# Optimization experiments

Measured on AMD Instinct MI355X. Metric: run time of the kernel, lower is better.

## Reference

```python
import jax, jax.numpy as jnp
import numpy as np

H, D = 2, 64          # heads, hidden_dim per head
HD = H * D            # 128
N_NODES = 50000
N_EDGES = 800000
N_GRAPHS = 64
IN_CH, EDGE_DIM, N_CLASSES = 2, 1, 30


def _tconv(x, src, dst, Wq, bq, Wk, bk, Wv, bv, We, Ws, bs):
    """PyG TransformerConv (concat=True, root_weight=True, beta=False)."""
    n = x.shape[0]
    q = (x @ Wq + bq).reshape(n, H, D)
    k = (x @ Wk + bk).reshape(n, H, D)
    v = (x @ Wv + bv).reshape(n, H, D)
    # edge embedding (lin_edge has no bias in PyG)
    return _attend(q, k, v, x @ Ws + bs, src, dst, We, n)


def _attend(q, k, v, skip, src, dst, We_e, n):
    kj = k[src] + We_e            # [E,H,D]
    vj = v[src] + We_e
    logits = (q[dst] * kj).sum(-1) / jnp.sqrt(jnp.asarray(D, q.dtype))  # [E,H]
    m = jax.ops.segment_max(logits, dst, num_segments=n)
    m = jnp.where(jnp.isfinite(m), m, jnp.zeros_like(m))
    ex = jnp.exp(logits - m[dst])
    denom = jax.ops.segment_sum(ex, dst, num_segments=n)
    alpha = ex / (denom[dst] + 1e-16)                                   # segment softmax
    agg = jax.ops.segment_sum(alpha[..., None] * vj, dst, num_segments=n)
    return agg.reshape(n, HD) + skip


def _forward(x, edge_index, edge_attr, batch,
             l0_Wq, l0_bq, l0_Wk, l0_bk, l0_Wv, l0_bv, l0_We, l0_Ws, l0_bs,
             l1_Wq, l1_bq, l1_Wk, l1_bk, l1_Wv, l1_bv, l1_We, l1_Ws, l1_bs,
             cW1, cb1, cW2, cb2):
    src, dst = edge_index[0], edge_index[1]
    e0 = (edge_attr @ l0_We).reshape(-1, H, D)
    e1 = (edge_attr @ l1_We).reshape(-1, H, D)
    n = x.shape[0]

    h = _attend((x @ l0_Wq + l0_bq).reshape(n, H, D),
                (x @ l0_Wk + l0_bk).reshape(n, H, D),
                (x @ l0_Wv + l0_bv).reshape(n, H, D),
                x @ l0_Ws + l0_bs, src, dst, e0, n)
    h = jax.nn.relu(h)
    h = _attend((h @ l1_Wq + l1_bq).reshape(n, H, D),
                (h @ l1_Wk + l1_bk).reshape(n, H, D),
                (h @ l1_Wv + l1_bv).reshape(n, H, D),
                h @ l1_Ws + l1_bs, src, dst, e1, n)
    h = jax.nn.relu(h)

    # global_mean_pool over graphs
    sums = jax.ops.segment_sum(h, batch, num_segments=N_GRAPHS)
    cnt = jax.ops.segment_sum(jnp.ones((n,), h.dtype), batch, num_segments=N_GRAPHS)
    g = sums / jnp.maximum(cnt, 1.0)[:, None]                           # [G, 128]

    return jax.nn.relu(g @ cW1 + cb1) @ cW2 + cb2                       # [G, 30]


def setup_inputs() -> dict:
    key = jax.random.key(0)
    ks = jax.random.split(key, 40)
    it = iter(ks)

    def lin(k, fan_in, fan_out):
        s = 1.0 / np.sqrt(fan_in)
        return jax.random.uniform(k, (fan_in, fan_out), jnp.float32, -s, s)

    inp = {
        'x': jax.random.normal(next(it), (N_NODES, IN_CH), jnp.float32),
        'edge_index': jax.random.randint(next(it), (2, N_EDGES), 0, N_NODES),
        'edge_attr': jax.random.normal(next(it), (N_EDGES, EDGE_DIM), jnp.float32),
        'batch': jnp.sort(jax.random.randint(next(it), (N_NODES,), 0, N_GRAPHS)),
    }
    for li, cin in (('l0', IN_CH), ('l1', HD)):
        for nm in ('Wq', 'Wk', 'Wv'):
            inp[f'{li}_{nm}'] = lin(next(it), cin, HD)
            inp[f'{li}_{nm.replace("W", "b")}'] = jax.random.uniform(
                next(it), (HD,), jnp.float32, -1 / np.sqrt(cin), 1 / np.sqrt(cin))
        inp[f'{li}_We'] = lin(next(it), EDGE_DIM, HD)
        inp[f'{li}_Ws'] = lin(next(it), cin, HD)
        inp[f'{li}_bs'] = jax.random.uniform(next(it), (HD,), jnp.float32,
                                             -1 / np.sqrt(cin), 1 / np.sqrt(cin))
    inp['cW1'] = lin(next(it), HD, 128)
    inp['cb1'] = jax.random.uniform(next(it), (128,), jnp.float32, -1 / np.sqrt(HD), 1 / np.sqrt(HD))
    inp['cW2'] = lin(next(it), 128, N_CLASSES)
    inp['cb2'] = jax.random.uniform(next(it), (N_CLASSES,), jnp.float32, -1 / np.sqrt(128), 1 / np.sqrt(128))
    return inp


def reference(x, edge_index, edge_attr, batch,
              l0_Wq, l0_bq, l0_Wk, l0_bk, l0_Wv, l0_bv, l0_We, l0_Ws, l0_bs,
              l1_Wq, l1_bq, l1_Wk, l1_bk, l1_Wv, l1_bv, l1_We, l1_Ws, l1_bs,
              cW1, cb1, cW2, cb2):
    return _forward(x, edge_index, edge_attr, batch,
                    l0_Wq, l0_bq, l0_Wk, l0_bk, l0_Wv, l0_bv, l0_We, l0_Ws, l0_bs,
                    l1_Wq, l1_bq, l1_Wk, l1_bk, l1_Wv, l1_bv, l1_We, l1_Ws, l1_bs,
                    cW1, cb1, cW2, cb2)
```

## Files before the change

### kernel.cpp

```cpp
#include <hip/hip_runtime.h>
#include <hip/hip_fp16.h>
#include <cstdint>
#include <cstddef>

#define HD 128

typedef short bf16x8 __attribute__((ext_vector_type(8)));
typedef float f32x4 __attribute__((ext_vector_type(4)));
typedef _Float16 h2f __attribute__((ext_vector_type(2)));

__device__ __forceinline__ h2f bits_to_h2(int v) {
    union { int i; h2f h; } u; u.i = v; return u.h;
}

#if __has_builtin(__builtin_amdgcn_fdot2)
#define DOT2(a, b) __builtin_amdgcn_fdot2((a), (b), 0.f, false)
#else
#define DOT2(a, b) fmaf((float)(a).x, (float)(b).x, (float)(a).y * (float)(b).y)
#endif

__device__ __forceinline__ unsigned short f2bf(float f) {
    unsigned int u = __float_as_uint(f);
    u += 0x7fff + ((u >> 16) & 1);
    return (unsigned short)(u >> 16);
}
__device__ __forceinline__ float bf2f(unsigned short h) {
    return __uint_as_float(((unsigned int)h) << 16);
}

template<int CTRL>
__device__ __forceinline__ float dpp_add(float x) {
    int y = __builtin_amdgcn_update_dpp(0, __float_as_int(x), CTRL, 0xF, 0xF, true);
    return x + __int_as_float(y);
}
__device__ __forceinline__ float half_reduce(float x) {
    x = dpp_add<0xB1>(x);
    x = dpp_add<0x4E>(x);
    x = dpp_add<0x124>(x);
    x = dpp_add<0x128>(x);
    x += __shfl_xor(x, 16, 64);
    return x;
}
__device__ __forceinline__ float wave_reduce(float x) {
    x = half_reduce(x);
    x += __shfl_xor(x, 32, 64);
    return x;
}

__device__ __forceinline__ void edge_pair(
    float& m, float& s, float& Sea, float2& acc, float cqwe, h2f q,
    int2 rawA, float aA, int2 rawB, float aB)
{
    h2f kA = bits_to_h2(rawA.x), vA = bits_to_h2(rawA.y);
    h2f kB = bits_to_h2(rawB.x), vB = bits_to_h2(rawB.y);
    float lA = fmaf(aA, cqwe, half_reduce(DOT2(q, kA)));
    float lB = fmaf(aB, cqwe, half_reduce(DOT2(q, kB)));
    float nm = fmaxf(fmaxf(m, lA), lB);
    float sc = __expf(m - nm);
    float eA = __expf(lA - nm);
    float eB = __expf(lB - nm);
    s   = fmaf(s, sc, eA + eB);
    Sea = fmaf(Sea, sc, fmaf(eA, aA, eB * aB));
    acc.x = fmaf(acc.x, sc, fmaf(eA, (float)vA.x, eB * (float)vB.x));
    acc.y = fmaf(acc.y, sc, fmaf(eA, (float)vA.y, eB * (float)vB.y));
    m = nm;
}
__device__ __forceinline__ void edge_single(
    float& m, float& s, float& Sea, float2& acc, float cqwe, h2f q,
    int2 rawA, float aA)
{
    h2f kA = bits_to_h2(rawA.x), vA = bits_to_h2(rawA.y);
    float lg = fmaf(aA, cqwe, half_reduce(DOT2(q, kA)));
    float nm = fmaxf(m, lg);
    float sc = __expf(m - nm);
    float ex = __expf(lg - nm);
    s   = fmaf(s, sc, ex);
    Sea = fmaf(Sea, sc, ex * aA);
    acc.x = fmaf(acc.x, sc, ex * (float)vA.x);
    acc.y = fmaf(acc.y, sc, ex * (float)vA.y);
    m = nm;
}

__global__ __launch_bounds__(256) void hist_kernel(
    const int* __restrict__ dst, int* __restrict__ cnt, int E)
{
    int e = blockIdx.x * 256 + threadIdx.x;
    if (e < E) atomicAdd(&cnt[dst[e]], 1);
}

__global__ __launch_bounds__(256) void scanA_kernel(
    const int* __restrict__ cnt, int* __restrict__ row_ptr,
    int* __restrict__ bsum, int n)
{
    __shared__ int sdata[256];
    int t = threadIdx.x;
    int base = blockIdx.x * 512 + 2 * t;
    int a = (base < n) ? cnt[base] : 0;
    int b = (base + 1 < n) ? cnt[base + 1] : 0;
    int local = a + b;
    sdata[t] = local;
    __syncthreads();
    #pragma unroll
    for (int off = 1; off < 256; off <<= 1) {
        int val = (t >= off) ? sdata[t - off] : 0;
        __syncthreads();
        sdata[t] += val;
        __syncthreads();
    }
    int excl = sdata[t] - local;
    if (base < n)     row_ptr[base] = excl;
    if (base + 1 < n) row_ptr[base + 1] = excl + a;
    if (t == 255) bsum[blockIdx.x] = sdata[255];
}

__global__ __launch_bounds__(256) void scanB_kernel(
    const int* __restrict__ bsum, int* __restrict__ boff, int B)
{
    __shared__ int sdata[256];
    int t = threadIdx.x;
    int local = (t < B) ? bsum[t] : 0;
    sdata[t] = local;
    __syncthreads();
    #pragma unroll
    for (int off = 1; off < 256; off <<= 1) {
        int val = (t >= off) ? sdata[t - off] : 0;
        __syncthreads();
        sdata[t] += val;
        __syncthreads();
    }
    if (t < B) boff[t] = sdata[t] - local;
}

__global__ __launch_bounds__(256) void scanC_kernel(
    int* __restrict__ row_ptr, int* __restrict__ cursor,
    const int* __restrict__ boff, int n, int E)
{
    int t = threadIdx.x;
    int base = blockIdx.x * 512 + 2 * t;
    int off = boff[blockIdx.x];
    if (base + 1 < n) {
        int2 v = *(int2*)&row_ptr[base];
        v.x += off; v.y += off;
        *(int2*)&row_ptr[base] = v;
        *(int2*)&cursor[base]  = v;
    } else if (base < n) {
        int v = row_ptr[base] + off;
        row_ptr[base] = v; cursor[base] = v;
    }
    if (blockIdx.x == 0 && t == 0) row_ptr[n] = E;
}

__global__ __launch_bounds__(256) void scatter_kernel(
    const int* __restrict__ dst, const int* __restrict__ src,
    const float* __restrict__ eattr, int* __restrict__ cursor,
    int2* __restrict__ epack, int E)
{
    int e = blockIdx.x * 256 + threadIdx.x;
    if (e < E) {
        int pos = atomicAdd(&cursor[dst[e]], 1);
        epack[pos] = make_int2(src[e], __float_as_int(eattr[e]));
    }
}

__global__ __launch_bounds__(128) void coef0_kernel(
    const float* __restrict__ Wq, const float* __restrict__ bq,
    const float* __restrict__ Wk, const float* __restrict__ bk,
    const float* __restrict__ We, float* __restrict__ coef)
{
    int w = threadIdx.x >> 6, l = threadIdx.x & 63;
    int j = w * 64 + l;
    float q0 = Wq[j], q1 = Wq[HD + j], qb = bq[j];
    float kv[4] = {Wk[j], Wk[HD + j], bk[j], We[j]};
    #pragma unroll
    for (int t = 0; t < 4; ++t) {
        float m0 = wave_reduce(kv[t] * q0);
        float m1 = wave_reduce(kv[t] * q1);
        float m2 = wave_reduce(kv[t] * qb);
        if (l == 0) {
            coef[w * 12 + t * 3 + 0] = m0 * 0.125f;
            coef[w * 12 + t * 3 + 1] = m1 * 0.125f;
            coef[w * 12 + t * 3 + 2] = m2 * 0.125f;
        }
    }
}

__global__ __launch_bounds__(256) void attn0a_kernel(
    const float* __restrict__ x, const float* __restrict__ coef,
    const int2* __restrict__ epack, const int* __restrict__ row_ptr,
    float4* __restrict__ S, int n)
{
    int i = blockIdx.x * 256 + threadIdx.x;
    if (i >= n) return;
    float C[24];
    #pragma unroll
    for (int t = 0; t < 24; ++t) C[t] = coef[t];
    float x0 = x[2 * i], x1 = x[2 * i + 1];
    float c0A = fmaf(x1, C[1],  fmaf(x0, C[0],  C[2]));
    float c1A = fmaf(x1, C[4],  fmaf(x0, C[3],  C[5]));
    float cbA = fmaf(x1, C[7],  fmaf(x0, C[6],  C[8]));
    float cwA = fmaf(x1, C[10], fmaf(x0, C[9],  C[11]));
    float c0B = fmaf(x1, C[13], fmaf(x0, C[12], C[14]));
    float c1B = fmaf(x1, C[16], fmaf(x0, C[15], C[17]));
    float cbB = fmaf(x1, C[19], fmaf(x0, C[18], C[20]));
    float cwB = fmaf(x1, C[22], fmaf(x0, C[21], C[23]));

    int p0 = row_ptr[i], p1 = row_ptr[i + 1];
    float mA = -INFINITY, sA = 0.f, SxA = 0.f, SyA = 0.f, SeA = 0.f;
    float mB = -INFINITY, sB = 0.f, SxB = 0.f, SyB = 0.f, SeB = 0.f;

    int2 epn = (p0 < p1) ? epack[p0] : make_int2(0, 0);
    for (int p = p0; p < p1; ++p) {
        int2 ep = epn;
        if (p + 1 < p1) epn = epack[p + 1];
        float ea = __int_as_float(ep.y);
        float2 xs = *(const float2*)&x[2 * ep.x];
        float lgA = fmaf(ea, cwA, fmaf(xs.y, c1A, fmaf(xs.x, c0A, cbA)));
        float lgB = fmaf(ea, cwB, fmaf(xs.y, c1B, fmaf(xs.x, c0B, cbB)));
        {
            float nm = fmaxf(mA, lgA);
            float sc = __expf(mA - nm);
            float ex = __expf(lgA - nm);
            sA  = fmaf(sA,  sc, ex);
            SxA = fmaf(SxA, sc, ex * xs.x);
            SyA = fmaf(SyA, sc, ex * xs.y);
            SeA = fmaf(SeA, sc, ex * ea);
            mA = nm;
        }
        {
            float nm = fmaxf(mB, lgB);
            float sc = __expf(mB - nm);
            float ex = __expf(lgB - nm);
            sB  = fmaf(sB,  sc, ex);
            SxB = fmaf(SxB, sc, ex * xs.x);
            SyB = fmaf(SyB, sc, ex * xs.y);
            SeB = fmaf(SeB, sc, ex * ea);
            mB = nm;
        }
    }
    S[(size_t)i * 2]     = make_float4(sA, SxA, SyA, SeA);
    S[(size_t)i * 2 + 1] = make_float4(sB, SxB, SyB, SeB);
}

__global__ __launch_bounds__(256) void attn_kernel(
    const __half* __restrict__ qh, const __half* __restrict__ kvh,
    const __half* __restrict__ sh, const float* __restrict__ We,
    const int2* __restrict__ epack, const int* __restrict__ row_ptr,
    __half2* __restrict__ outh, int n)
{
    int i = blockIdx.x * 4 + (threadIdx.x >> 6);
    if (i >= n) return;
    int l = threadIdx.x & 63;
    const int2* kv8 = (const int2*)kvh;
    const int* qraw = (const int*)qh;
    const __half2* sh2 = (const __half2*)sh;
    h2f q = bits_to_h2(qraw[(size_t)i * 64 + l]);
    float2 we = *(const float2*)&We[2 * l];
    float cqwe = half_reduce(fmaf((float)q.x, we.x, (float)q.y * we.y));
    int p0 = __builtin_amdgcn_readfirstlane(row_ptr[i]);
    int p1 = __builtin_amdgcn_readfirstlane(row_ptr[i + 1]);

    float m = -INFINITY, s = 0.f, Sea = 0.f;
    float2 acc = make_float2(0.f, 0.f);

    int2 kv0 = {}, kv1 = {}, kv2 = {}, kv3 = {};
    float ea0 = 0.f, ea1 = 0.f, ea2 = 0.f, ea3 = 0.f;

#define LD1(t, idx) do { if ((idx) < p1) { int2 ep_ = epack[idx]; \
    ea##t = __int_as_float(ep_.y); kv##t = kv8[(size_t)ep_.x * 64 + l]; } } while (0)

    LD1(0, p0); LD1(1, p0 + 1); LD1(2, p0 + 2); LD1(3, p0 + 3);

    int p = p0;
    for (; p + 3 < p1; p += 4) {
        int2 c0 = kv0, c1 = kv1, c2 = kv2, c3 = kv3;
        float a0 = ea0, a1 = ea1, a2 = ea2, a3 = ea3;
        LD1(0, p + 4); LD1(1, p + 5); LD1(2, p + 6); LD1(3, p + 7);
        edge_pair(m, s, Sea, acc, cqwe, q, c0, a0, c1, a1);
        edge_pair(m, s, Sea, acc, cqwe, q, c2, a2, c3, a3);
    }
    int rem = p1 - p;
    if (rem >= 2) edge_pair(m, s, Sea, acc, cqwe, q, kv0, ea0, kv1, ea1);
    if (rem == 1)      edge_single(m, s, Sea, acc, cqwe, q, kv0, ea0);
    else if (rem == 3) edge_single(m, s, Sea, acc, cqwe, q, kv2, ea2);

    float inv = 1.f / (s + 1e-16f);
    float2 skp = __half22float2(sh2[(size_t)i * 64 + l]);
    float rx = fmaxf(fmaf(fmaf(Sea, we.x, acc.x), inv, skp.x), 0.f);
    float ry = fmaxf(fmaf(fmaf(Sea, we.y, acc.y), inv, skp.y), 0.f);
    outh[(size_t)i * 64 + l] = __floats2half2_rn(rx, ry);
}

__global__ __launch_bounds__(256) void pack_kernel(
    const float* __restrict__ Wq, const float* __restrict__ Wk,
    const float* __restrict__ Wv, const float* __restrict__ Ws,
    const float* __restrict__ bq, const float* __restrict__ bk,
    const float* __restrict__ bv, const float* __restrict__ bs,
    unsigned short* __restrict__ Wph, unsigned short* __restrict__ Wpl,
    float* __restrict__ bias_cat)
{
    int id = blockIdx.x * 256 + threadIdx.x;
    if (id < 65536) {
        int j = id & 7, lane = (id >> 3) & 63, ks = (id >> 9) & 3, gnt = id >> 11;
        int k = ks * 32 + (lane >> 4) * 8 + j;
        int ncol = gnt * 16 + (lane & 15);
        int mat = ncol >> 7, d = ncol & 127;
        const float* W = (mat == 0) ? Wq : (mat == 1) ? Wk : (mat == 2) ? Wv : Ws;
        float w = W[k * HD + d];
        unsigned short hi = f2bf(w);
        Wph[id] = hi;
        Wpl[id] = f2bf(w - bf2f(hi));
    }
    if (id < 512) {
        int mat = id >> 7, d = id & 127;
        const float* b = (mat == 0) ? bq : (mat == 1) ? bk : (mat == 2) ? bv : bs;
        bias_cat[id] = b[d];
    }
}

__global__ __launch_bounds__(256) void lin1_mfma(
    const float* __restrict__ x, const float4* __restrict__ S0,
    const float* __restrict__ l0Wv, const float* __restrict__ l0bv,
    const float* __restrict__ l0We,
    const float* __restrict__ l0Ws, const float* __restrict__ l0bs,
    const unsigned short* __restrict__ Wph, const unsigned short* __restrict__ Wpl,
    const float* __restrict__ bias_cat,
    __half* __restrict__ qh, __half* __restrict__ kvh, __half* __restrict__ sh,
    int n)
{
    __shared__ float As[128 * 128];
    int tid = threadIdx.x;
    int row0 = blockIdx.x * 128;

    {
        int c4 = tid & 31;
        int c0 = c4 * 4;
        int rb = tid >> 5;
        int hh = c4 >> 4;
        float4 wv0 = *(const float4*)&l0Wv[c0];
        float4 wv1 = *(const float4*)&l0Wv[HD + c0];
        float4 bv4 = *(const float4*)&l0bv[c0];
        float4 we4 = *(const float4*)&l0We[c0];
        float4 ws0 = *(const float4*)&l0Ws[c0];
        float4 ws1 = *(const float4*)&l0Ws[HD + c0];
        float4 bs4 = *(const float4*)&l0bs[c0];
        #pragma unroll
        for (int it = 0; it < 16; ++it) {
            int r = it * 8 + rb;
            float4 av = make_float4(0.f, 0.f, 0.f, 0.f);
            if (row0 + r < n) {
                float2 xr = *(const float2*)&x[2 * (size_t)(row0 + r)];
                float4 Sv = S0[(size_t)(row0 + r) * 2 + hh];
                float inv = 1.f / (Sv.x + 1e-16f);
                float n0 = fmaf(wv0.x, Sv.y, fmaf(wv1.x, Sv.z, fmaf(bv4.x, Sv.x, we4.x * Sv.w)));
                float n1 = fmaf(wv0.y, Sv.y, fmaf(wv1.y, Sv.z, fmaf(bv4.y, Sv.x, we4.y * Sv.w)));
                float n2 = fmaf(wv0.z, Sv.y, fmaf(wv1.z, Sv.z, fmaf(bv4.z, Sv.x, we4.z * Sv.w)));
                float n3 = fmaf(wv0.w, Sv.y, fmaf(wv1.w, Sv.z, fmaf(bv4.w, Sv.x, we4.w * Sv.w)));
                av.x = fmaxf(fmaf(n0, inv, fmaf(xr.y, ws1.x, fmaf(xr.x, ws0.x, bs4.x))), 0.f);
                av.y = fmaxf(fmaf(n1, inv, fmaf(xr.y, ws1.y, fmaf(xr.x, ws0.y, bs4.y))), 0.f);
                av.z = fmaxf(fmaf(n2, inv, fmaf(xr.y, ws1.z, fmaf(xr.x, ws0.z, bs4.z))), 0.f);
                av.w = fmaxf(fmaf(n3, inv, fmaf(xr.y, ws1.w, fmaf(xr.x, ws0.w, bs4.w))), 0.f);
            }
            int sl = c4 ^ (r & 7);
            *(float4*)&As[r * 128 + sl * 4] = av;
        }
    }
    __syncthreads();

    int wave = tid >> 6, lane = tid & 63;
    int m = lane & 15, quad = lane >> 4;

    bf16x8 ah[2][4], al[2][4];
    #pragma unroll
    for (int sub = 0; sub < 2; ++sub) {
        int r = wave * 32 + sub * 16 + m;
        const float* base = &As[r * 128];
        int sw = r & 7;
        #pragma unroll
        for (int ks = 0; ks < 4; ++ks) {
            int i40 = (ks * 8 + quad * 2) ^ sw;
            int i41 = (ks * 8 + quad * 2 + 1) ^ sw;
            float4 x0 = *(const float4*)&base[i40 * 4];
            float4 x1 = *(const float4*)&base[i41 * 4];
            float v[8] = {x0.x, x0.y, x0.z, x0.w, x1.x, x1.y, x1.z, x1.w};
            #pragma unroll
            for (int j = 0; j < 8; ++j) {
                unsigned short hi = f2bf(v[j]);
                ah[sub][ks][j] = (short)hi;
                al[sub][ks][j] = (short)f2bf(v[j] - bf2f(hi));
            }
        }
    }
    __syncthreads();

    const bf16x8* PH = (const bf16x8*)Wph;
    const bf16x8* PL = (const bf16x8*)Wpl;
    __half2* qh2 = (__half2*)qh;
    __half2* sh2 = (__half2*)sh;
    __half*  kvS = (__half*)As;

    bf16x8 bhA[4], blA[4], bhB[4], blB[4];
    #pragma unroll
    for (int ks = 0; ks < 4; ++ks) {
        bhA[ks] = PH[ks * 64 + lane];
        blA[ks] = PL[ks * 64 + lane];
    }

    for (int gnt = 0; gnt < 32; ++gnt) {
        if (gnt + 1 < 32) {
            #pragma unroll
            for (int ks = 0; ks < 4; ++ks) {
                bhB[ks] = PH[((gnt + 1) * 4 + ks) * 64 + lane];
                blB[ks] = PL[((gnt + 1) * 4 + ks) * 64 + lane];
            }
        }
        f32x4 acc0 = {0.f, 0.f, 0.f, 0.f};
        f32x4 acc1 = {0.f, 0.f, 0.f, 0.f};
        #pragma unroll
        for (int ks = 0; ks < 4; ++ks) {
            acc0 = __builtin_amdgcn_mfma_f32_16x16x32_bf16(ah[0][ks], bhA[ks], acc0, 0, 0, 0);
            acc1 = __builtin_amdgcn_mfma_f32_16x16x32_bf16(ah[1][ks], bhA[ks], acc1, 0, 0, 0);
            acc0 = __builtin_amdgcn_mfma_f32_16x16x32_bf16(ah[0][ks], blA[ks], acc0, 0, 0, 0);
            acc1 = __builtin_amdgcn_mfma_f32_16x16x32_bf16(ah[1][ks], blA[ks], acc1, 0, 0, 0);
            acc0 = __builtin_amdgcn_mfma_f32_16x16x32_bf16(al[0][ks], bhA[ks], acc0, 0, 0, 0);
            acc1 = __builtin_amdgcn_mfma_f32_16x16x32_bf16(al[1][ks], bhA[ks], acc1, 0, 0, 0);
        }
        int ocol = gnt * 16 + m;
        int d = ocol & 127;
        float bias = bias_cat[ocol];
        bool iskv = (gnt >= 8) && (gnt < 24);
        if (!iskv) {
            bool isq = (gnt < 8);
            __half2* dst = isq ? qh2 : sh2;
            float osc = isq ? 0.125f : 1.0f;
            bool evenl = (m & 1) == 0;
            #pragma unroll
            for (int sub = 0; sub < 2; ++sub) {
                f32x4 acc = sub ? acc1 : acc0;
                #pragma unroll
                for (int reg = 0; reg < 4; ++reg) {
                    int orow = row0 + wave * 32 + sub * 16 + quad * 4 + reg;
                    float val = (acc[reg] + bias) * osc;
                    float other = __shfl_xor(val, 1, 64);
                    if (orow < n && evenl)
                        dst[(size_t)orow * 64 + (d >> 1)] = __floats2half2_rn(val, other);
                }
            }
        } else {
            int slot = 4 * (d >> 1) + (d & 1) + ((gnt >= 16) ? 2 : 0);
            #pragma unroll
            for (int sub = 0; sub < 2; ++sub) {
                f32x4 acc = sub ? acc1 : acc0;
                #pragma unroll
                for (int reg = 0; reg < 4; ++reg) {
                    int row_l = wave * 32 + sub * 16 + quad * 4 + reg;
                    kvS[row_l * 256 + slot] = __float2half(acc[reg] + bias);
                }
            }
        }
        #pragma unroll
        for (int ks = 0; ks < 4; ++ks) { bhA[ks] = bhB[ks]; blA[ks] = blB[ks]; }
    }

    __syncthreads();
    const float4* kvS4 = (const float4*)kvS;
    float4* kvh4 = (float4*)kvh;
    #pragma unroll
    for (int it = 0; it < 16; ++it) {
        int idx = it * 256 + tid;
        int row = idx >> 5, c4 = idx & 31;
        if (row0 + row < n)
            kvh4[(size_t)(row0 + row) * 32 + c4] = kvS4[row * 32 + c4];
    }
}

__global__ __launch_bounds__(128) void pool_kernel(
    const __half* __restrict__ h, const int* __restrict__ batch,
    float* __restrict__ gsums, int n)
{
    __shared__ int sb[64];
    int i0 = blockIdx.x * 64;
    int d = threadIdx.x;
    int iend = i0 + 64; if (iend > n) iend = n;
    int csize = iend - i0;
    if (d < csize) sb[d] = batch[i0 + d];
    __syncthreads();
    if (csize <= 0) return;
    float local = 0.f;
    int cur = sb[0];
    for (int i = i0; i < iend; ++i) {
        int g = sb[i - i0];
        if (g != cur) {
            atomicAdd(&gsums[(size_t)cur * HD + d], local);
            local = 0.f; cur = g;
        }
        local += __half2float(h[(size_t)i * HD + d]);
    }
    atomicAdd(&gsums[(size_t)cur * HD + d], local);
}

__global__ __launch_bounds__(128) void cls_kernel(
    const float* __restrict__ gsums, const int* __restrict__ batch,
    const float* __restrict__ cW1, const float* __restrict__ cb1,
    const float* __restrict__ cW2, const float* __restrict__ cb2,
    float* __restrict__ out, int n)
{
    __shared__ float g[128];
    __shared__ float t[128];
    int gi = blockIdx.x, j = threadIdx.x;
    int lo = 0, hi = n;
    while (lo < hi) { int mid = (lo + hi) >> 1; if (batch[mid] < gi) lo = mid + 1; else hi = mid; }
    int start = lo;
    lo = start; hi = n;
    while (lo < hi) { int mid = (lo + hi) >> 1; if (batch[mid] < gi + 1) lo = mid + 1; else hi = mid; }
    float c = fmaxf((float)(lo - start), 1.0f);
    g[j] = gsums[(size_t)gi * HD + j] / c;
    __syncthreads();
    float a = cb1[j];
    for (int k = 0; k < 128; ++k) a = fmaf(g[k], cW1[k * 128 + j], a);
    t[j] = fmaxf(a, 0.f);
    __syncthreads();
    if (j < 30) {
        float a2 = cb2[j];
        for (int k = 0; k < 128; ++k) a2 = fmaf(t[k], cW2[k * 30 + j], a2);
        out[gi * 30 + j] = a2;
    }
}

extern "C" void kernel_launch(void* const* d_in, const int* in_sizes, int n_in,
                              void* d_out, int out_size, void* d_ws, size_t ws_size,
                              hipStream_t stream)
{
    const float* x     = (const float*)d_in[0];
    const int*   ei    = (const int*)d_in[1];
    const float* eattr = (const float*)d_in[2];
    const int*   batch = (const int*)d_in[3];
    const float* l0_Wq = (const float*)d_in[4];
    const float* l0_bq = (const float*)d_in[5];
    const float* l0_Wk = (const float*)d_in[6];
    const float* l0_bk = (const float*)d_in[7];
    const float* l0_Wv = (const float*)d_in[8];
    const float* l0_bv = (const float*)d_in[9];
    const float* l0_We = (const float*)d_in[10];
    const float* l0_Ws = (const float*)d_in[11];
    const float* l0_bs = (const float*)d_in[12];
    const float* l1_Wq = (const float*)d_in[13];
    const float* l1_bq = (const float*)d_in[14];
    const float* l1_Wk = (const float*)d_in[15];
    const float* l1_bk = (const float*)d_in[16];
    const float* l1_Wv = (const float*)d_in[17];
    const float* l1_bv = (const float*)d_in[18];
    const float* l1_We = (const float*)d_in[19];
    const float* l1_Ws = (const float*)d_in[20];
    const float* l1_bs = (const float*)d_in[21];
    const float* cW1   = (const float*)d_in[22];
    const float* cb1   = (const float*)d_in[23];
    const float* cW2   = (const float*)d_in[24];
    const float* cb2   = (const float*)d_in[25];

    int n = in_sizes[0] / 2;
    int E = in_sizes[2];
    int G = out_size / 30;
    int B = (n + 511) / 512;

    size_t nd = (size_t)n * HD;
    __half* h1    = (__half*)d_ws;
    __half* qh    = h1 + nd;
    __half* sh    = qh + nd;
    __half* kvh   = sh + nd;
    float* bias_cat = (float*)(kvh + (size_t)n * 256);
    unsigned short* Wph = (unsigned short*)(bias_cat + 512);
    unsigned short* Wpl = Wph + 65536;
    float* coef   = (float*)(Wpl + 65536);
    float4* S0    = (float4*)(coef + 32);
    int2* epack   = (int2*)(S0 + (size_t)n * 2);
    int* cnt      = (int*)(epack + E);
    int* row_ptr  = cnt + n;
    int* cursor   = row_ptr + n + 2;
    int* bsum     = cursor + n;
    int* boff     = bsum + 256;
    float* gsums  = (float*)(boff + 256);

    const int* srcI = ei;
    const int* dstI = ei + E;

    hipMemsetAsync(cnt, 0, (size_t)n * sizeof(int), stream);
    hipMemsetAsync(gsums, 0, (size_t)G * HD * sizeof(float), stream);

    hist_kernel<<<(E + 255) / 256, 256, 0, stream>>>(dstI, cnt, E);
    scanA_kernel<<<B, 256, 0, stream>>>(cnt, row_ptr, bsum, n);
    scanB_kernel<<<1, 256, 0, stream>>>(bsum, boff, B);
    scanC_kernel<<<B, 256, 0, stream>>>(row_ptr, cursor, boff, n, E);
    scatter_kernel<<<(E + 255) / 256, 256, 0, stream>>>(dstI, srcI, eattr, cursor, epack, E);

    pack_kernel<<<256, 256, 0, stream>>>(l1_Wq, l1_Wk, l1_Wv, l1_Ws,
                                         l1_bq, l1_bk, l1_bv, l1_bs,
                                         Wph, Wpl, bias_cat);
    coef0_kernel<<<1, 128, 0, stream>>>(l0_Wq, l0_bq, l0_Wk, l0_bk, l0_We, coef);

    attn0a_kernel<<<(n + 255) / 256, 256, 0, stream>>>(
        x, coef, epack, row_ptr, S0, n);

    lin1_mfma<<<(n + 127) / 128, 256, 0, stream>>>(
        x, S0, l0_Wv, l0_bv, l0_We, l0_Ws, l0_bs,
        Wph, Wpl, bias_cat, qh, kvh, sh, n);
    attn_kernel<<<(n + 3) / 4, 256, 0, stream>>>(
        qh, kvh, sh, l1_We, epack, row_ptr, (__half2*)h1, n);

    pool_kernel<<<(n + 63) / 64, 128, 0, stream>>>(h1, batch, gsums, n);
    cls_kernel<<<G, 128, 0, stream>>>(gsums, batch, cW1, cb1, cW2, cb2,
                                      (float*)d_out, n);
}
```

Measured before the change: 359.6 us.

## Fuse setup kernels, split attn0a edges across lane pairs, shrink lin1 tile

Folds the coef0 computation, the cnt zeroing and the weight packing into one pack_kernel, and replaces both memsets. scanB is merged into scanC, with each block re-scanning the block sums itself. attn0a now gives each node two threads that walk alternate edges and merge their online-softmax states with shuffles, which raises parallelism for the low-occupancy gather loop. lin1_mfma uses 64-row tiles instead of 128, halving shared memory and doubling the grid for occupancy, and it zeroes gsums in block 0. The costs are redundant scan work per block and less MFMA reuse of the B fragments per tile.

```diff
diff --git a/kernel.cpp b/kernel.cpp
--- a/kernel.cpp
+++ b/kernel.cpp
@@ -81,6 +81,56 @@
     m = nm;
 }
 
+__global__ __launch_bounds__(256) void pack_kernel(
+    const float* __restrict__ Wq, const float* __restrict__ Wk,
+    const float* __restrict__ Wv, const float* __restrict__ Ws,
+    const float* __restrict__ bq, const float* __restrict__ bk,
+    const float* __restrict__ bv, const float* __restrict__ bs,
+    const float* __restrict__ l0Wq, const float* __restrict__ l0bq,
+    const float* __restrict__ l0Wk, const float* __restrict__ l0bk,
+    const float* __restrict__ l0We,
+    unsigned short* __restrict__ Wph, unsigned short* __restrict__ Wpl,
+    float* __restrict__ bias_cat, float* __restrict__ coef,
+    int* __restrict__ cnt, int n)
+{
+    int tid = threadIdx.x;
+    int id = blockIdx.x * 256 + tid;
+    if (id < 65536) {
+        int j = id & 7, lane = (id >> 3) & 63, ks = (id >> 9) & 3, gnt = id >> 11;
+        int k = ks * 32 + (lane >> 4) * 8 + j;
+        int ncol = gnt * 16 + (lane & 15);
+        int mat = ncol >> 7, d = ncol & 127;
+        const float* W = (mat == 0) ? Wq : (mat == 1) ? Wk : (mat == 2) ? Wv : Ws;
+        float w = W[k * HD + d];
+        unsigned short hi = f2bf(w);
+        Wph[id] = hi;
+        Wpl[id] = f2bf(w - bf2f(hi));
+    }
+    if (id < 512) {
+        int mat = id >> 7, d = id & 127;
+        const float* b = (mat == 0) ? bq : (mat == 1) ? bk : (mat == 2) ? bv : bs;
+        bias_cat[id] = b[d];
+    }
+    if (id < n) cnt[id] = 0;
+    if (blockIdx.x == 256 && tid < 128) {
+        int w = tid >> 6, l = tid & 63;
+        int j = w * 64 + l;
+        float q0 = l0Wq[j], q1 = l0Wq[HD + j], qb = l0bq[j];
+        float kv[4] = {l0Wk[j], l0Wk[HD + j], l0bk[j], l0We[j]};
+        #pragma unroll
+        for (int t = 0; t < 4; ++t) {
+            float m0 = wave_reduce(kv[t] * q0);
+            float m1 = wave_reduce(kv[t] * q1);
+            float m2 = wave_reduce(kv[t] * qb);
+            if (l == 0) {
+                coef[w * 12 + t * 3 + 0] = m0 * 0.125f;
+                coef[w * 12 + t * 3 + 1] = m1 * 0.125f;
+                coef[w * 12 + t * 3 + 2] = m2 * 0.125f;
+            }
+        }
+    }
+}
+
 __global__ __launch_bounds__(256) void hist_kernel(
     const int* __restrict__ dst, int* __restrict__ cnt, int E)
 {
@@ -113,12 +163,13 @@
     if (t == 255) bsum[blockIdx.x] = sdata[255];
 }
 
-__global__ __launch_bounds__(256) void scanB_kernel(
-    const int* __restrict__ bsum, int* __restrict__ boff, int B)
+__global__ __launch_bounds__(256) void scanC_kernel(
+    int* __restrict__ row_ptr, int* __restrict__ cursor,
+    const int* __restrict__ bsum, int n, int E, int B)
 {
     __shared__ int sdata[256];
     int t = threadIdx.x;
-    int local = (t < B) ? bsum[t] : 0;
+    int local = (t < B && t < (int)blockIdx.x) ? bsum[t] : 0;
     sdata[t] = local;
     __syncthreads();
     #pragma unroll
@@ -128,16 +179,8 @@
         sdata[t] += val;
         __syncthreads();
     }
-    if (t < B) boff[t] = sdata[t] - local;
-}
-
-__global__ __launch_bounds__(256) void scanC_kernel(
-    int* __restrict__ row_ptr, int* __restrict__ cursor,
-    const int* __restrict__ boff, int n, int E)
-{
-    int t = threadIdx.x;
+    int off = sdata[255];
     int base = blockIdx.x * 512 + 2 * t;
-    int off = boff[blockIdx.x];
     if (base + 1 < n) {
         int2 v = *(int2*)&row_ptr[base];
         v.x += off; v.y += off;
@@ -162,34 +205,13 @@
     }
 }
 
-__global__ __launch_bounds__(128) void coef0_kernel(
-    const float* __restrict__ Wq, const float* __restrict__ bq,
-    const float* __restrict__ Wk, const float* __restrict__ bk,
-    const float* __restrict__ We, float* __restrict__ coef)
-{
-    int w = threadIdx.x >> 6, l = threadIdx.x & 63;
-    int j = w * 64 + l;
-    float q0 = Wq[j], q1 = Wq[HD + j], qb = bq[j];
-    float kv[4] = {Wk[j], Wk[HD + j], bk[j], We[j]};
-    #pragma unroll
-    for (int t = 0; t < 4; ++t) {
-        float m0 = wave_reduce(kv[t] * q0);
-        float m1 = wave_reduce(kv[t] * q1);
-        float m2 = wave_reduce(kv[t] * qb);
-        if (l == 0) {
-            coef[w * 12 + t * 3 + 0] = m0 * 0.125f;
-            coef[w * 12 + t * 3 + 1] = m1 * 0.125f;
-            coef[w * 12 + t * 3 + 2] = m2 * 0.125f;
-        }
-    }
-}
-
 __global__ __launch_bounds__(256) void attn0a_kernel(
     const float* __restrict__ x, const float* __restrict__ coef,
     const int2* __restrict__ epack, const int* __restrict__ row_ptr,
     float4* __restrict__ S, int n)
 {
-    int i = blockIdx.x * 256 + threadIdx.x;
+    int gid = blockIdx.x * 256 + threadIdx.x;
+    int i = gid >> 1, pr = gid & 1;
     if (i >= n) return;
     float C[24];
     #pragma unroll
@@ -208,10 +230,11 @@
     float mA = -INFINITY, sA = 0.f, SxA = 0.f, SyA = 0.f, SeA = 0.f;
     float mB = -INFINITY, sB = 0.f, SxB = 0.f, SyB = 0.f, SeB = 0.f;
 
-    int2 epn = (p0 < p1) ? epack[p0] : make_int2(0, 0);
-    for (int p = p0; p < p1; ++p) {
+    int p = p0 + pr;
+    int2 epn = (p < p1) ? epack[p] : make_int2(0, 0);
+    for (; p < p1; p += 2) {
         int2 ep = epn;
-        if (p + 1 < p1) epn = epack[p + 1];
+        if (p + 2 < p1) epn = epack[p + 2];
         float ea = __int_as_float(ep.y);
         float2 xs = *(const float2*)&x[2 * ep.x];
         float lgA = fmaf(ea, cwA, fmaf(xs.y, c1A, fmaf(xs.x, c0A, cbA)));
@@ -237,8 +260,30 @@
             mB = nm;
         }
     }
-    S[(size_t)i * 2]     = make_float4(sA, SxA, SyA, SeA);
-    S[(size_t)i * 2 + 1] = make_float4(sB, SxB, SyB, SeB);
+    {
+        float mO = __shfl_xor(mA, 1, 64);
+        float mM = fmaxf(mA, mO);
+        float e = (mA > -INFINITY) ? __expf(mA - mM) : 0.f;
+        sA *= e; SxA *= e; SyA *= e; SeA *= e;
+        sA  += __shfl_xor(sA, 1, 64);
+        SxA += __shfl_xor(SxA, 1, 64);
+        SyA += __shfl_xor(SyA, 1, 64);
+        SeA += __shfl_xor(SeA, 1, 64);
+    }
+    {
+        float mO = __shfl_xor(mB, 1, 64);
+        float mM = fmaxf(mB, mO);
+        float e = (mB > -INFINITY) ? __expf(mB - mM) : 0.f;
+        sB *= e; SxB *= e; SyB *= e; SeB *= e;
+        sB  += __shfl_xor(sB, 1, 64);
+        SxB += __shfl_xor(SxB, 1, 64);
+        SyB += __shfl_xor(SyB, 1, 64);
+        SeB += __shfl_xor(SeB, 1, 64);
+    }
+    if (pr == 0) {
+        S[(size_t)i * 2]     = make_float4(sA, SxA, SyA, SeA);
+        S[(size_t)i * 2 + 1] = make_float4(sB, SxB, SyB, SeB);
+    }
 }
 
 __global__ __launch_bounds__(256) void attn_kernel(
@@ -290,33 +335,6 @@
     outh[(size_t)i * 64 + l] = __floats2half2_rn(rx, ry);
 }
 
-__global__ __launch_bounds__(256) void pack_kernel(
-    const float* __restrict__ Wq, const float* __restrict__ Wk,
-    const float* __restrict__ Wv, const float* __restrict__ Ws,
-    const float* __restrict__ bq, const float* __restrict__ bk,
-    const float* __restrict__ bv, const float* __restrict__ bs,
-    unsigned short* __restrict__ Wph, unsigned short* __restrict__ Wpl,
-    float* __restrict__ bias_cat)
-{
-    int id = blockIdx.x * 256 + threadIdx.x;
-    if (id < 65536) {
-        int j = id & 7, lane = (id >> 3) & 63, ks = (id >> 9) & 3, gnt = id >> 11;
-        int k = ks * 32 + (lane >> 4) * 8 + j;
-        int ncol = gnt * 16 + (lane & 15);
-        int mat = ncol >> 7, d = ncol & 127;
-        const float* W = (mat == 0) ? Wq : (mat == 1) ? Wk : (mat == 2) ? Wv : Ws;
-        float w = W[k * HD + d];
-        unsigned short hi = f2bf(w);
-        Wph[id] = hi;
-        Wpl[id] = f2bf(w - bf2f(hi));
-    }
-    if (id < 512) {
-        int mat = id >> 7, d = id & 127;
-        const float* b = (mat == 0) ? bq : (mat == 1) ? bk : (mat == 2) ? bv : bs;
-        bias_cat[id] = b[d];
-    }
-}
-
 __global__ __launch_bounds__(256) void lin1_mfma(
     const float* __restrict__ x, const float4* __restrict__ S0,
     const float* __restrict__ l0Wv, const float* __restrict__ l0bv,
@@ -325,11 +343,15 @@
     const unsigned short* __restrict__ Wph, const unsigned short* __restrict__ Wpl,
     const float* __restrict__ bias_cat,
     __half* __restrict__ qh, __half* __restrict__ kvh, __half* __restrict__ sh,
-    int n)
-{
-    __shared__ float As[128 * 128];
+    float* __restrict__ gsums, int gn, int n)
+{
+    __shared__ float As[64 * 128];
     int tid = threadIdx.x;
-    int row0 = blockIdx.x * 128;
+    int row0 = blockIdx.x * 64;
+
+    if (blockIdx.x == 0) {
+        for (int k = tid; k < gn; k += 256) gsums[k] = 0.f;
+    }
 
     {
         int c4 = tid & 31;
@@ -344,7 +366,7 @@
         float4 ws1 = *(const float4*)&l0Ws[HD + c0];
         float4 bs4 = *(const float4*)&l0bs[c0];
         #pragma unroll
-        for (int it = 0; it < 16; ++it) {
+        for (int it = 0; it < 8; ++it) {
             int r = it * 8 + rb;
             float4 av = make_float4(0.f, 0.f, 0.f, 0.f);
             if (row0 + r < n) {
@@ -369,10 +391,9 @@
     int wave = tid >> 6, lane = tid & 63;
     int m = lane & 15, quad = lane >> 4;
 
-    bf16x8 ah[2][4], al[2][4];
-    #pragma unroll
-    for (int sub = 0; sub < 2; ++sub) {
-        int r = wave * 32 + sub * 16 + m;
+    bf16x8 ah[4], al[4];
+    {
+        int r = wave * 16 + m;
         const float* base = &As[r * 128];
         int sw = r & 7;
         #pragma unroll
@@ -385,8 +406,8 @@
             #pragma unroll
             for (int j = 0; j < 8; ++j) {
                 unsigned short hi = f2bf(v[j]);
-                ah[sub][ks][j] = (short)hi;
-                al[sub][ks][j] = (short)f2bf(v[j] - bf2f(hi));
+                ah[ks][j] = (short)hi;
+                al[ks][j] = (short)f2bf(v[j] - bf2f(hi));
             }
         }
     }
@@ -413,16 +434,12 @@
                 blB[ks] = PL[((gnt + 1) * 4 + ks) * 64 + lane];
             }
         }
-        f32x4 acc0 = {0.f, 0.f, 0.f, 0.f};
-        f32x4 acc1 = {0.f, 0.f, 0.f, 0.f};
+        f32x4 acc = {0.f, 0.f, 0.f, 0.f};
         #pragma unroll
         for (int ks = 0; ks < 4; ++ks) {
-            acc0 = __builtin_amdgcn_mfma_f32_16x16x32_bf16(ah[0][ks], bhA[ks], acc0, 0, 0, 0);
-            acc1 = __builtin_amdgcn_mfma_f32_16x16x32_bf16(ah[1][ks], bhA[ks], acc1, 0, 0, 0);
-            acc0 = __builtin_amdgcn_mfma_f32_16x16x32_bf16(ah[0][ks], blA[ks], acc0, 0, 0, 0);
-            acc1 = __builtin_amdgcn_mfma_f32_16x16x32_bf16(ah[1][ks], blA[ks], acc1, 0, 0, 0);
-            acc0 = __builtin_amdgcn_mfma_f32_16x16x32_bf16(al[0][ks], bhA[ks], acc0, 0, 0, 0);
-            acc1 = __builtin_amdgcn_mfma_f32_16x16x32_bf16(al[1][ks], bhA[ks], acc1, 0, 0, 0);
+            acc = __builtin_amdgcn_mfma_f32_16x16x32_bf16(ah[ks], bhA[ks], acc, 0, 0, 0);
+            acc = __builtin_amdgcn_mfma_f32_16x16x32_bf16(ah[ks], blA[ks], acc, 0, 0, 0);
+            acc = __builtin_amdgcn_mfma_f32_16x16x32_bf16(al[ks], bhA[ks], acc, 0, 0, 0);
         }
         int ocol = gnt * 16 + m;
         int d = ocol & 127;
@@ -434,27 +451,19 @@
             float osc = isq ? 0.125f : 1.0f;
             bool evenl = (m & 1) == 0;
             #pragma unroll
-            for (int sub = 0; sub < 2; ++sub) {
-                f32x4 acc = sub ? acc1 : acc0;
-                #pragma unroll
-                for (int reg = 0; reg < 4; ++reg) {
-                    int orow = row0 + wave * 32 + sub * 16 + quad * 4 + reg;
-                    float val = (acc[reg] + bias) * osc;
-                    float other = __shfl_xor(val, 1, 64);
-                    if (orow < n && evenl)
-                        dst[(size_t)orow * 64 + (d >> 1)] = __floats2half2_rn(val, other);
-                }
+            for (int reg = 0; reg < 4; ++reg) {
+                int orow = row0 + wave * 16 + quad * 4 + reg;
+                float val = (acc[reg] + bias) * osc;
+                float other = __shfl_xor(val, 1, 64);
+                if (orow < n && evenl)
+                    dst[(size_t)orow * 64 + (d >> 1)] = __floats2half2_rn(val, other);
             }
         } else {
             int slot = 4 * (d >> 1) + (d & 1) + ((gnt >= 16) ? 2 : 0);
             #pragma unroll
-            for (int sub = 0; sub < 2; ++sub) {
-                f32x4 acc = sub ? acc1 : acc0;
-                #pragma unroll
-                for (int reg = 0; reg < 4; ++reg) {
-                    int row_l = wave * 32 + sub * 16 + quad * 4 + reg;
-                    kvS[row_l * 256 + slot] = __float2half(acc[reg] + bias);
-                }
+            for (int reg = 0; reg < 4; ++reg) {
+                int row_l = wave * 16 + quad * 4 + reg;
+                kvS[row_l * 256 + slot] = __float2half(acc[reg] + bias);
             }
         }
         #pragma unroll
@@ -465,7 +474,7 @@
     const float4* kvS4 = (const float4*)kvS;
     float4* kvh4 = (float4*)kvh;
     #pragma unroll
-    for (int it = 0; it < 16; ++it) {
+    for (int it = 0; it < 8; ++it) {
         int idx = it * 256 + tid;
         int row = idx >> 5, c4 = idx & 31;
         if (row0 + row < n)
@@ -577,32 +586,26 @@
     int* row_ptr  = cnt + n;
     int* cursor   = row_ptr + n + 2;
     int* bsum     = cursor + n;
-    int* boff     = bsum + 256;
-    float* gsums  = (float*)(boff + 256);
+    float* gsums  = (float*)(bsum + 256);
 
     const int* srcI = ei;
     const int* dstI = ei + E;
 
-    hipMemsetAsync(cnt, 0, (size_t)n * sizeof(int), stream);
-    hipMemsetAsync(gsums, 0, (size_t)G * HD * sizeof(float), stream);
-
+    pack_kernel<<<257, 256, 0, stream>>>(l1_Wq, l1_Wk, l1_Wv, l1_Ws,
+                                         l1_bq, l1_bk, l1_bv, l1_bs,
+                                         l0_Wq, l0_bq, l0_Wk, l0_bk, l0_We,
+                                         Wph, Wpl, bias_cat, coef, cnt, n);
     hist_kernel<<<(E + 255) / 256, 256, 0, stream>>>(dstI, cnt, E);
     scanA_kernel<<<B, 256, 0, stream>>>(cnt, row_ptr, bsum, n);
-    scanB_kernel<<<1, 256, 0, stream>>>(bsum, boff, B);
-    scanC_kernel<<<B, 256, 0, stream>>>(row_ptr, cursor, boff, n, E);
+    scanC_kernel<<<B, 256, 0, stream>>>(row_ptr, cursor, bsum, n, E, B);
     scatter_kernel<<<(E + 255) / 256, 256, 0, stream>>>(dstI, srcI, eattr, cursor, epack, E);
 
-    pack_kernel<<<256, 256, 0, stream>>>(l1_Wq, l1_Wk, l1_Wv, l1_Ws,
-                                         l1_bq, l1_bk, l1_bv, l1_bs,
-                                         Wph, Wpl, bias_cat);
-    coef0_kernel<<<1, 128, 0, stream>>>(l0_Wq, l0_bq, l0_Wk, l0_bk, l0_We, coef);
-
-    attn0a_kernel<<<(n + 255) / 256, 256, 0, stream>>>(
+    attn0a_kernel<<<(2 * n + 255) / 256, 256, 0, stream>>>(
         x, coef, epack, row_ptr, S0, n);
 
-    lin1_mfma<<<(n + 127) / 128, 256, 0, stream>>>(
+    lin1_mfma<<<(n + 63) / 64, 256, 0, stream>>>(
         x, S0, l0_Wv, l0_bv, l0_We, l0_Ws, l0_bs,
-        Wph, Wpl, bias_cat, qh, kvh, sh, n);
+        Wph, Wpl, bias_cat, qh, kvh, sh, gsums, G * HD, n);
     attn_kernel<<<(n + 3) / 4, 256, 0, stream>>>(
         qh, kvh, sh, l1_We, epack, row_ptr, (__half2*)h1, n);
 
```

Result: no change. 357.9 us (-0.5%).
